# Kernel optimization log

Measured on AMD Instinct MI355X. Metric: run time of the kernel, lower is better.

## Reference

```python
import jax, jax.numpy as jnp
import numpy as np

T, B, E, H = 2048, 2, 1024, 16
D = E // H
NEG = -1e18


def setup_inputs() -> dict:
    key = jax.random.key(0)
    k1, k2, k3, k4, k5 = jax.random.split(key, 5)
    return {
        "query": jax.random.normal(k1, (T, B, E), dtype=jnp.float32),
        "in_proj_weight": jax.random.normal(k2, (3 * E, E), dtype=jnp.float32) * 0.02,
        "in_proj_bias": jax.random.normal(k3, (3 * E,), dtype=jnp.float32) * 0.02,
        "out_proj_weight": jax.random.normal(k4, (E, E), dtype=jnp.float32) * 0.02,
        "out_proj_bias": jax.random.normal(k5, (E,), dtype=jnp.float32) * 0.02,
    }


def reference(query, in_proj_weight, in_proj_bias, out_proj_weight, out_proj_bias):
    # Self-attention (qkv_same), mask_future_timesteps=True, no padding mask,
    # eval mode (dropout p=0), need_weights=True.
    tgt_len, bsz, embed_dim = query.shape
    # fused in-projection: [T,B,3E]
    qkv = jnp.einsum("tbe,fe->tbf", query, in_proj_weight) + in_proj_bias
    q, k, v = jnp.split(qkv, 3, axis=-1)
    q = q * (D ** -0.5)
    # [T,B,E] -> [B*H, T, D]
    def to_heads(x):
        return x.reshape(tgt_len, bsz * H, D).transpose(1, 0, 2)
    q, k, v = to_heads(q), to_heads(k), to_heads(v)
    # scores: [B*H, T, T]
    scores = jnp.einsum("ntd,nsd->nts", q, k)
    causal = jnp.triu(jnp.full((tgt_len, tgt_len), NEG, dtype=scores.dtype), k=1)
    scores = scores + causal[None, :, :]
    attn_weights = jax.nn.softmax(scores, axis=-1)
    # context: [B*H, T, D] -> [T, B, E]
    ctx = jnp.einsum("nts,nsd->ntd", attn_weights, v)
    ctx = ctx.transpose(1, 0, 2).reshape(tgt_len, bsz, embed_dim)
    out = jnp.einsum("tbe,fe->tbf", ctx, out_proj_weight) + out_proj_bias
    # averaged attention weights over heads: [B, T, T]
    avg_w = attn_weights.reshape(bsz, H, tgt_len, tgt_len).sum(axis=1) / H
    return (out, avg_w)
```

## Files before the change

kernel.cpp:

```cpp
#include <hip/hip_runtime.h>
#include <math.h>

#define T_LEN 2048
#define BSZ 2
#define EMB 1024
#define NHEAD 16
#define HDIM 64
#define QK_LD 2048

typedef __attribute__((ext_vector_type(8))) short short8v;
typedef __attribute__((ext_vector_type(4))) float floatx4;

__device__ __forceinline__ short f2bf(float f) {
    unsigned u = __float_as_uint(f);
    u += 0x7fffu + ((u >> 16) & 1u);
    return (short)(u >> 16);
}

__device__ __forceinline__ void async16(const short* g, short* l) {
    __builtin_amdgcn_global_load_lds(
        (const __attribute__((address_space(1))) void*)g,
        (__attribute__((address_space(3))) void*)l, 16, 0, 0);
}

__global__ __launch_bounds__(256) void f32_to_bf16_k(const float* __restrict__ src,
                                                     short* __restrict__ dst, int n) {
    int i = (blockIdx.x * 256 + threadIdx.x) * 4;
    if (i >= n) return;
    float4 v = *(const float4*)(src + i);
    short4 o = make_short4(f2bf(v.x), f2bf(v.y), f2bf(v.z), f2bf(v.w));
    *(short4*)(dst + i) = o;
}

__global__ __launch_bounds__(256) void gemm_bf16(const short* __restrict__ A,
        const short* __restrict__ B, const float* __restrict__ bias,
        void* __restrict__ Cout, short* __restrict__ vTout,
        int M, int N, int K, int scale_cols, int out_bf16, int ldC) {
    __shared__ short As[128][32];
    __shared__ short Bs[128][32];
    const int tid = threadIdx.x;
    const int m0 = blockIdx.x * 128, n0 = blockIdx.y * 128;
    const int lane = tid & 63, w = tid >> 6;
    const int q = lane >> 4, r = lane & 15;
    const int wr = w >> 1, wc = w & 1;

    const int srow = lane >> 2;
    const int spos = lane & 3;
    const int rowL = w * 16 + srow;
    const int rowH = 64 + rowL;
    const int csrc = spos ^ ((rowL >> 1) & 3);
    const short* gA0 = A + (size_t)(m0 + rowL) * K + csrc * 8;
    const short* gA1 = A + (size_t)(m0 + rowH) * K + csrc * 8;
    const short* gB0 = B + (size_t)(n0 + rowL) * K + csrc * 8;
    const short* gB1 = B + (size_t)(n0 + rowH) * K + csrc * 8;
    short* lA0 = &As[w * 16][0];
    short* lA1 = &As[64 + w * 16][0];
    short* lB0 = &Bs[w * 16][0];
    short* lB1 = &Bs[64 + w * 16][0];

    floatx4 acc[4][4];
    #pragma unroll
    for (int a = 0; a < 4; ++a)
        #pragma unroll
        for (int b2 = 0; b2 < 4; ++b2)
            #pragma unroll
            for (int e = 0; e < 4; ++e) acc[a][b2][e] = 0.f;

    for (int k0 = 0; k0 < K; k0 += 32) {
        __syncthreads();
        async16(gA0 + k0, lA0);
        async16(gA1 + k0, lA1);
        async16(gB0 + k0, lB0);
        async16(gB1 + k0, lB1);
        __syncthreads();
        short8v af[4], bfr[4];
        #pragma unroll
        for (int mb = 0; mb < 4; ++mb) {
            int row = wr * 64 + mb * 16 + r;
            af[mb] = *(const short8v*)&As[row][(q ^ ((row >> 1) & 3)) * 8];
        }
        #pragma unroll
        for (int nb = 0; nb < 4; ++nb) {
            int row = wc * 64 + nb * 16 + r;
            bfr[nb] = *(const short8v*)&Bs[row][(q ^ ((row >> 1) & 3)) * 8];
        }
        #pragma unroll
        for (int mb = 0; mb < 4; ++mb)
            #pragma unroll
            for (int nb = 0; nb < 4; ++nb)
                acc[mb][nb] = __builtin_amdgcn_mfma_f32_16x16x32_bf16(af[mb], bfr[nb], acc[mb][nb], 0, 0, 0);
    }

    #pragma unroll
    for (int nb = 0; nb < 4; ++nb) {
        const int col = n0 + wc * 64 + nb * 16 + r;
        const float bi = bias[col];
        const float sc = (col < scale_cols) ? 0.125f : 1.0f;
        if (vTout && col >= 2 * EMB) {
            const int e = col - 2 * EMB;
            #pragma unroll
            for (int mb = 0; mb < 4; ++mb) {
                const int base = m0 + wr * 64 + mb * 16 + q * 4;
                float v0 = acc[mb][nb][0] + bi, v1 = acc[mb][nb][1] + bi;
                float v2 = acc[mb][nb][2] + bi, v3 = acc[mb][nb][3] + bi;
                unsigned lo = (unsigned short)f2bf(v0) | ((unsigned)(unsigned short)f2bf(v2) << 16);
                unsigned hi = (unsigned short)f2bf(v1) | ((unsigned)(unsigned short)f2bf(v3) << 16);
                *(unsigned*)&vTout[(size_t)e * T_LEN + (base >> 1)]         = lo;
                *(unsigned*)&vTout[((size_t)EMB + e) * T_LEN + (base >> 1)] = hi;
            }
        } else {
            #pragma unroll
            for (int mb = 0; mb < 4; ++mb)
                #pragma unroll
                for (int i = 0; i < 4; ++i) {
                    const int rowg = m0 + wr * 64 + mb * 16 + q * 4 + i;
                    const float v = (acc[mb][nb][i] + bi) * sc;
                    if (out_bf16) ((short*)Cout)[(size_t)rowg * ldC + col] = f2bf(v);
                    else          ((float*)Cout)[(size_t)rowg * ldC + col] = v;
                }
        }
    }
}

__global__ __launch_bounds__(256) void flash_fwd(const short* __restrict__ qk,
        const short* __restrict__ vT, short* __restrict__ ctx,
        float* __restrict__ Lr) {
    __shared__ short Ks[128][64];
    __shared__ short Vt[64][128];
    __shared__ short Ps[2][64][64];
    __shared__ float Lred[4][64];
    const int tid = threadIdx.x;
    const int bh = blockIdx.x;
    const int tt = 31 - blockIdx.y;
    const int t0 = tt << 6;
    const int b = bh >> 4, h = bh & 15;
    const int lane = tid & 63, w = tid >> 6;
    const int q = lane >> 4, r = lane & 15;
    const int RS = BSZ * QK_LD;

    const short* qbase = qk + (size_t)b * QK_LD + h * HDIM;
    const short* kbase = qbase + EMB;
    const short* vbase = vT + ((size_t)b * EMB + h * HDIM) * T_LEN;

    const int krow0 = w * 32 + (lane >> 3);
    const short* kg = kbase + (size_t)krow0 * RS + ((lane & 7) ^ (krow0 & 7)) * 8;
    const int vrow0 = w * 16 + (lane >> 4);
    const short* vg[4];
    #pragma unroll
    for (int j = 0; j < 4; ++j) {
        const int vr = vrow0 + j * 4;
        const int gc = ((lane & 15) & 8) | (((lane & 15) & 7) ^ (vr & 7));
        vg[j] = vbase + (size_t)vr * T_LEN + gc * 8;
    }

    {
        const int sr = tid >> 3, c8 = tid & 7;
        *(int4*)&Ps[0][sr][(c8 ^ (sr & 7)) * 8] =
            *(const int4*)(qbase + (size_t)(t0 + sr) * RS + c8 * 8);
        *(int4*)&Ps[0][sr + 32][(c8 ^ ((sr + 32) & 7)) * 8] =
            *(const int4*)(qbase + (size_t)(t0 + sr + 32) * RS + c8 * 8);
    }
    __syncthreads();
    short8v qf[4][2];
    #pragma unroll
    for (int mb = 0; mb < 4; ++mb)
        #pragma unroll
        for (int ks = 0; ks < 2; ++ks) {
            int row = mb * 16 + r;
            qf[mb][ks] = *(const short8v*)&Ps[0][row][((ks * 4 + q) ^ (row & 7)) * 8];
        }

    float l_part[4][4];
    floatx4 o[4];
    #pragma unroll
    for (int mb = 0; mb < 4; ++mb)
        #pragma unroll
        for (int i = 0; i < 4; ++i) l_part[mb][i] = 0.f;
    #pragma unroll
    for (int nb = 0; nb < 4; ++nb)
        #pragma unroll
        for (int e = 0; e < 4; ++e) o[nb][e] = 0.f;

    const int ntiles = tt + 1;
    int s2 = 0;
    for (; s2 + 2 <= ntiles; s2 += 2) {
        __syncthreads();
        {
            const short* kgr = kg + (size_t)(s2 * 64) * RS;
            #pragma unroll
            for (int j = 0; j < 4; ++j)
                async16(kgr + (size_t)(j * 8) * RS, &Ks[w * 32 + j * 8][0]);
            #pragma unroll
            for (int j = 0; j < 4; ++j)
                async16(vg[j] + s2 * 64, &Vt[w * 16 + j * 4][0]);
        }
        __syncthreads();
        #pragma unroll
        for (int t2 = 0; t2 < 2; ++t2) {
            floatx4 sf[4];
            #pragma unroll
            for (int mb = 0; mb < 4; ++mb)
                #pragma unroll
                for (int e = 0; e < 4; ++e) sf[mb][e] = 0.f;
            #pragma unroll
            for (int ks = 0; ks < 2; ++ks) {
                const int krow = t2 * 64 + w * 16 + r;
                short8v kf = *(const short8v*)&Ks[krow][((ks * 4 + q) ^ (krow & 7)) * 8];
                #pragma unroll
                for (int mb = 0; mb < 4; ++mb)
                    sf[mb] = __builtin_amdgcn_mfma_f32_16x16x32_bf16(qf[mb][ks], kf, sf[mb], 0, 0, 0);
            }
            const bool diag = (s2 + t2 == tt);
            #pragma unroll
            for (int mb = 0; mb < 4; ++mb)
                #pragma unroll
                for (int i = 0; i < 4; ++i) {
                    const int rl = mb * 16 + q * 4 + i;
                    float p = (diag && (w * 16 + r > rl)) ? 0.f : __expf(sf[mb][i]);
                    l_part[mb][i] += p;
                    const int c = (w * 2 + (r >> 3)) ^ (rl & 7);
                    Ps[t2][rl][c * 8 + (r & 7)] = f2bf(p);
                }
        }
        __syncthreads();
        #pragma unroll
        for (int ks = 0; ks < 2; ++ks) {
            const int prow = w * 16 + r;
            const int pcp = ((ks * 4 + q) ^ (prow & 7)) * 8;
            short8v pfA = *(const short8v*)&Ps[0][prow][pcp];
            short8v pfB = *(const short8v*)&Ps[1][prow][pcp];
            #pragma unroll
            for (int nb = 0; nb < 4; ++nb) {
                const int vrow = nb * 16 + r;
                const int pcv = (ks * 4 + q) ^ (vrow & 7);
                short8v vfA = *(const short8v*)&Vt[vrow][pcv * 8];
                short8v vfB = *(const short8v*)&Vt[vrow][(8 | pcv) * 8];
                o[nb] = __builtin_amdgcn_mfma_f32_16x16x32_bf16(pfA, vfA, o[nb], 0, 0, 0);
                o[nb] = __builtin_amdgcn_mfma_f32_16x16x32_bf16(pfB, vfB, o[nb], 0, 0, 0);
            }
        }
    }
    if (s2 < ntiles) {
        __syncthreads();
        {
            const int sr = tid >> 2, cb = (tid & 3) * 2;
            const short* kp = kbase + (size_t)(s2 * 64 + sr) * RS;
            const short* vp = vbase + (size_t)sr * T_LEN + s2 * 64;
            #pragma unroll
            for (int u = 0; u < 2; ++u) {
                const int c = cb + u;
                *(int4*)&Ks[sr][(c ^ (sr & 7)) * 8] = *(const int4*)(kp + c * 8);
                *(int4*)&Vt[sr][(c ^ (sr & 7)) * 8] = *(const int4*)(vp + c * 8);
            }
        }
        __syncthreads();
        floatx4 sf[4];
        #pragma unroll
        for (int mb = 0; mb < 4; ++mb)
            #pragma unroll
            for (int e = 0; e < 4; ++e) sf[mb][e] = 0.f;
        #pragma unroll
        for (int ks = 0; ks < 2; ++ks) {
            const int krow = w * 16 + r;
            short8v kf = *(const short8v*)&Ks[krow][((ks * 4 + q) ^ (krow & 7)) * 8];
            #pragma unroll
            for (int mb = 0; mb < 4; ++mb)
                sf[mb] = __builtin_amdgcn_mfma_f32_16x16x32_bf16(qf[mb][ks], kf, sf[mb], 0, 0, 0);
        }
        #pragma unroll
        for (int mb = 0; mb < 4; ++mb)
            #pragma unroll
            for (int i = 0; i < 4; ++i) {
                const int rl = mb * 16 + q * 4 + i;
                float p = (w * 16 + r > rl) ? 0.f : __expf(sf[mb][i]);
                l_part[mb][i] += p;
                const int c = (w * 2 + (r >> 3)) ^ (rl & 7);
                Ps[0][rl][c * 8 + (r & 7)] = f2bf(p);
            }
        __syncthreads();
        #pragma unroll
        for (int ks = 0; ks < 2; ++ks) {
            const int prow = w * 16 + r;
            short8v pf = *(const short8v*)&Ps[0][prow][((ks * 4 + q) ^ (prow & 7)) * 8];
            #pragma unroll
            for (int nb = 0; nb < 4; ++nb) {
                const int vrow = nb * 16 + r;
                short8v vf = *(const short8v*)&Vt[vrow][(((ks * 4 + q) ^ (vrow & 7))) * 8];
                o[nb] = __builtin_amdgcn_mfma_f32_16x16x32_bf16(pf, vf, o[nb], 0, 0, 0);
            }
        }
    }

    #pragma unroll
    for (int mb = 0; mb < 4; ++mb)
        #pragma unroll
        for (int i = 0; i < 4; ++i) {
            float v = l_part[mb][i];
            v += __shfl_xor(v, 1, 16);
            v += __shfl_xor(v, 2, 16);
            v += __shfl_xor(v, 4, 16);
            v += __shfl_xor(v, 8, 16);
            if (r == 0) Lred[w][mb * 16 + q * 4 + i] = v;
        }
    __syncthreads();
    if (tid < 64) {
        float s = Lred[0][tid] + Lred[1][tid] + Lred[2][tid] + Lred[3][tid];
        Lr[(size_t)bh * T_LEN + t0 + tid] = s;
        Lred[0][tid] = s;
    }
    __syncthreads();
    #pragma unroll
    for (int i = 0; i < 4; ++i) {
        const int tl = w * 16 + q * 4 + i;
        const float inv = 1.0f / Lred[0][tl];
        #pragma unroll
        for (int nb = 0; nb < 4; ++nb)
            ctx[((size_t)(t0 + tl) * BSZ + b) * EMB + h * HDIM + nb * 16 + r] =
                f2bf(o[nb][i] * inv);
    }
}

__global__ __launch_bounds__(256) void avg_w_k(const short* __restrict__ qk,
        const float* __restrict__ Lr, float* __restrict__ avg) {
    const int s0 = blockIdx.x * 64, t0 = blockIdx.y * 64, b = blockIdx.z;
    const int tid = threadIdx.x;
    float* outb = avg + (size_t)b * T_LEN * T_LEN;
    if (s0 > t0) {
        const int ty = tid >> 4, tx = tid & 15;
        const float4 z = make_float4(0.f, 0.f, 0.f, 0.f);
        #pragma unroll
        for (int i = 0; i < 4; ++i)
            *(float4*)&outb[(size_t)(t0 + ty * 4 + i) * T_LEN + s0 + tx * 4] = z;
        return;
    }
    __shared__ short Qs[64][128];
    __shared__ short Ks[64][128];
    __shared__ float Lbuf[NHEAD][64];
    const int lane = tid & 63, w = tid >> 6;
    const int q = lane >> 4, r = lane & 15;
    const short* qbase = qk + (size_t)b * QK_LD;
    const int RS = BSZ * QK_LD;

    #pragma unroll
    for (int u = 0; u < 4; ++u) {
        const int li = tid * 4 + u;
        const int h = li >> 6, tl = li & 63;
        Lbuf[h][tl] = 0.0625f / Lr[(size_t)(b * NHEAD + h) * T_LEN + t0 + tl];
    }

    const short* qg[4]; const short* kg[4];
    #pragma unroll
    for (int j = 0; j < 4; ++j) {
        const int row = w * 16 + j * 4 + (lane >> 4);
        const int c = lane & 15;
        const int gc = (c & 8) | ((c & 7) ^ (row & 7));
        qg[j] = qbase + (size_t)(t0 + row) * RS + gc * 8;
        kg[j] = qbase + EMB + (size_t)(s0 + row) * RS + gc * 8;
    }

    floatx4 acc[4];
    #pragma unroll
    for (int nb = 0; nb < 4; ++nb)
        #pragma unroll
        for (int e = 0; e < 4; ++e) acc[nb][e] = 0.f;

    for (int hp = 0; hp < 8; ++hp) {
        __syncthreads();
        #pragma unroll
        for (int j = 0; j < 4; ++j)
            async16(qg[j] + hp * 128, &Qs[w * 16 + j * 4][0]);
        #pragma unroll
        for (int j = 0; j < 4; ++j)
            async16(kg[j] + hp * 128, &Ks[w * 16 + j * 4][0]);
        __syncthreads();

        #pragma unroll
        for (int hs = 0; hs < 2; ++hs) {
            const int h = hp * 2 + hs;
            floatx4 sf[4];
            #pragma unroll
            for (int nb = 0; nb < 4; ++nb)
                #pragma unroll
                for (int e = 0; e < 4; ++e) sf[nb][e] = 0.f;
            #pragma unroll
            for (int ks = 0; ks < 2; ++ks) {
                const int qrow = w * 16 + r;
                short8v qfr = *(const short8v*)
                    &Qs[qrow][((hs * 8) | ((ks * 4 + q) ^ (qrow & 7))) * 8];
                #pragma unroll
                for (int nb = 0; nb < 4; ++nb) {
                    const int krow = nb * 16 + r;
                    short8v kfr = *(const short8v*)
                        &Ks[krow][((hs * 8) | ((ks * 4 + q) ^ (krow & 7))) * 8];
                    sf[nb] = __builtin_amdgcn_mfma_f32_16x16x32_bf16(qfr, kfr, sf[nb], 0, 0, 0);
                }
            }
            #pragma unroll
            for (int i = 0; i < 4; ++i) {
                const int tl = w * 16 + q * 4 + i;
                const float inv = Lbuf[h][tl];
                #pragma unroll
                for (int nb = 0; nb < 4; ++nb) {
                    float e = (s0 == t0 && (nb * 16 + r > tl))
                              ? 0.f : __expf(sf[nb][i]) * inv;
                    acc[nb][i] += e;
                }
            }
        }
    }

    #pragma unroll
    for (int i = 0; i < 4; ++i) {
        const int t = t0 + w * 16 + q * 4 + i;
        #pragma unroll
        for (int nb = 0; nb < 4; ++nb)
            outb[(size_t)t * T_LEN + s0 + nb * 16 + r] = acc[nb][i];
    }
}

extern "C" void kernel_launch(void* const* d_in, const int* in_sizes, int n_in,
                              void* d_out, int out_size, void* d_ws, size_t ws_size,
                              hipStream_t stream) {
    (void)in_sizes; (void)n_in; (void)out_size; (void)ws_size;
    const float* query = (const float*)d_in[0];
    const float* w_in  = (const float*)d_in[1];
    const float* b_in  = (const float*)d_in[2];
    const float* w_out = (const float*)d_in[3];
    const float* b_out = (const float*)d_in[4];

    float* out = (float*)d_out;
    float* avg = out + (size_t)T_LEN * BSZ * EMB;

    short* ws     = (short*)d_ws;
    short* wb_in  = ws;
    short* wb_out = wb_in  + (size_t)3072 * 1024;
    short* qkb    = wb_out + (size_t)1024 * 1024;
    short* vTb    = qkb    + (size_t)4096 * 2048;
    short* ctxb   = vTb    + (size_t)BSZ * EMB * T_LEN;
    float* Lr     = (float*)(ctxb + (size_t)4096 * 1024);
    short* qb     = ctxb;

    f32_to_bf16_k<<<4096, 256, 0, stream>>>(query, qb,     4096 * 1024);
    f32_to_bf16_k<<<3072, 256, 0, stream>>>(w_in,  wb_in,  3072 * 1024);
    f32_to_bf16_k<<<1024, 256, 0, stream>>>(w_out, wb_out, 1024 * 1024);

    gemm_bf16<<<dim3(32, 24), 256, 0, stream>>>(qb, wb_in, b_in, qkb, vTb,
                                                4096, 3072, 1024, EMB, 1, QK_LD);
    flash_fwd<<<dim3(32, 32), 256, 0, stream>>>(qkb, vTb, ctxb, Lr);
    avg_w_k<<<dim3(32, 32, 2), 256, 0, stream>>>(qkb, Lr, avg);
    gemm_bf16<<<dim3(32, 8), 256, 0, stream>>>(ctxb, wb_out, b_out, out, (short*)0,
                                               4096, 1024, 1024, 0, 0, 1024);
}
```

Before: 236.1 us.

## Keep P in registers in flash attention via transposed S and split-K PV

The flash kernel now computes S transposed (K as the A operand) so each lane's score outputs form a ready bf16 A-fragment for a 16x16x16 MFMA with V. The probabilities no longer round-trip through shared memory, which removes the Ps buffer and one barrier per tile pair. Each wave now accumulates a partial O over its own key slice for all 64 query rows, so O registers grow fourfold and a cross-wave reduction through LDS is added at the end. The PV product also moves to smaller-K MFMA instructions, so more MFMA issues are needed per tile.

```diff
diff --git a/kernel.cpp b/kernel.cpp
--- a/kernel.cpp
+++ b/kernel.cpp
@@ -9,6 +9,7 @@
 #define QK_LD 2048
 
 typedef __attribute__((ext_vector_type(8))) short short8v;
+typedef __attribute__((ext_vector_type(4))) short short4v;
 typedef __attribute__((ext_vector_type(4))) float floatx4;
 
 __device__ __forceinline__ short f2bf(float f) {
@@ -16,6 +17,17 @@
     u += 0x7fffu + ((u >> 16) & 1u);
     return (short)(u >> 16);
 }
+
+#if __has_builtin(__builtin_amdgcn_mfma_f32_16x16x16bf16_1k)
+#define MFMA16(a, b, c) __builtin_amdgcn_mfma_f32_16x16x16bf16_1k(a, b, c, 0, 0, 0)
+#else
+__device__ __forceinline__ floatx4 mfma16_asm(short4v a, short4v b, floatx4 c) {
+    floatx4 d;
+    asm("v_mfma_f32_16x16x16_bf16 %0, %1, %2, %3" : "=v"(d) : "v"(a), "v"(b), "v"(c));
+    return d;
+}
+#define MFMA16(a, b, c) mfma16_asm(a, b, c)
+#endif
 
 __device__ __forceinline__ void async16(const short* g, short* l) {
     __builtin_amdgcn_global_load_lds(
@@ -125,9 +137,8 @@
 __global__ __launch_bounds__(256) void flash_fwd(const short* __restrict__ qk,
         const short* __restrict__ vT, short* __restrict__ ctx,
         float* __restrict__ Lr) {
-    __shared__ short Ks[128][64];
-    __shared__ short Vt[64][128];
-    __shared__ short Ps[2][64][64];
+    __shared__ __align__(16) short Ks[128][64];
+    __shared__ __align__(16) short Vt[64][128];
     __shared__ float Lred[4][64];
     const int tid = threadIdx.x;
     const int bh = blockIdx.x;
@@ -155,9 +166,9 @@
 
     {
         const int sr = tid >> 3, c8 = tid & 7;
-        *(int4*)&Ps[0][sr][(c8 ^ (sr & 7)) * 8] =
+        *(int4*)&Ks[sr][(c8 ^ (sr & 7)) * 8] =
             *(const int4*)(qbase + (size_t)(t0 + sr) * RS + c8 * 8);
-        *(int4*)&Ps[0][sr + 32][(c8 ^ ((sr + 32) & 7)) * 8] =
+        *(int4*)&Ks[sr + 32][(c8 ^ ((sr + 32) & 7)) * 8] =
             *(const int4*)(qbase + (size_t)(t0 + sr + 32) * RS + c8 * 8);
     }
     __syncthreads();
@@ -167,19 +178,19 @@
         #pragma unroll
         for (int ks = 0; ks < 2; ++ks) {
             int row = mb * 16 + r;
-            qf[mb][ks] = *(const short8v*)&Ps[0][row][((ks * 4 + q) ^ (row & 7)) * 8];
-        }
-
-    float l_part[4][4];
-    floatx4 o[4];
+            qf[mb][ks] = *(const short8v*)&Ks[row][((ks * 4 + q) ^ (row & 7)) * 8];
+        }
+
+    float l_part[4] = {0.f, 0.f, 0.f, 0.f};
+    floatx4 o[4][4];
     #pragma unroll
     for (int mb = 0; mb < 4; ++mb)
         #pragma unroll
-        for (int i = 0; i < 4; ++i) l_part[mb][i] = 0.f;
-    #pragma unroll
-    for (int nb = 0; nb < 4; ++nb)
-        #pragma unroll
-        for (int e = 0; e < 4; ++e) o[nb][e] = 0.f;
+        for (int nb = 0; nb < 4; ++nb)
+            #pragma unroll
+            for (int e = 0; e < 4; ++e) o[mb][nb][e] = 0.f;
+
+    const int voffbase = (((w * 2 + (q >> 1)) ^ (r & 7)) * 8) + (q & 1) * 4;
 
     const int ntiles = tt + 1;
     int s2 = 0;
@@ -197,46 +208,34 @@
         __syncthreads();
         #pragma unroll
         for (int t2 = 0; t2 < 2; ++t2) {
-            floatx4 sf[4];
-            #pragma unroll
-            for (int mb = 0; mb < 4; ++mb)
-                #pragma unroll
-                for (int e = 0; e < 4; ++e) sf[mb][e] = 0.f;
-            #pragma unroll
-            for (int ks = 0; ks < 2; ++ks) {
-                const int krow = t2 * 64 + w * 16 + r;
-                short8v kf = *(const short8v*)&Ks[krow][((ks * 4 + q) ^ (krow & 7)) * 8];
-                #pragma unroll
-                for (int mb = 0; mb < 4; ++mb)
-                    sf[mb] = __builtin_amdgcn_mfma_f32_16x16x32_bf16(qf[mb][ks], kf, sf[mb], 0, 0, 0);
-            }
+            const int krow = t2 * 64 + w * 16 + r;
+            const int ksw = krow & 7;
+            short8v kf0 = *(const short8v*)&Ks[krow][(q ^ ksw) * 8];
+            short8v kf1 = *(const short8v*)&Ks[krow][((4 + q) ^ ksw) * 8];
+            short4v vf[4];
+            #pragma unroll
+            for (int nb = 0; nb < 4; ++nb)
+                vf[nb] = *(const short4v*)&Vt[nb * 16 + r][t2 * 64 + voffbase];
             const bool diag = (s2 + t2 == tt);
             #pragma unroll
-            for (int mb = 0; mb < 4; ++mb)
-                #pragma unroll
-                for (int i = 0; i < 4; ++i) {
-                    const int rl = mb * 16 + q * 4 + i;
-                    float p = (diag && (w * 16 + r > rl)) ? 0.f : __expf(sf[mb][i]);
-                    l_part[mb][i] += p;
-                    const int c = (w * 2 + (r >> 3)) ^ (rl & 7);
-                    Ps[t2][rl][c * 8 + (r & 7)] = f2bf(p);
-                }
-        }
-        __syncthreads();
-        #pragma unroll
-        for (int ks = 0; ks < 2; ++ks) {
-            const int prow = w * 16 + r;
-            const int pcp = ((ks * 4 + q) ^ (prow & 7)) * 8;
-            short8v pfA = *(const short8v*)&Ps[0][prow][pcp];
-            short8v pfB = *(const short8v*)&Ps[1][prow][pcp];
-            #pragma unroll
-            for (int nb = 0; nb < 4; ++nb) {
-                const int vrow = nb * 16 + r;
-                const int pcv = (ks * 4 + q) ^ (vrow & 7);
-                short8v vfA = *(const short8v*)&Vt[vrow][pcv * 8];
-                short8v vfB = *(const short8v*)&Vt[vrow][(8 | pcv) * 8];
-                o[nb] = __builtin_amdgcn_mfma_f32_16x16x32_bf16(pfA, vfA, o[nb], 0, 0, 0);
-                o[nb] = __builtin_amdgcn_mfma_f32_16x16x32_bf16(pfB, vfB, o[nb], 0, 0, 0);
+            for (int mb = 0; mb < 4; ++mb) {
+                floatx4 sf;
+                #pragma unroll
+                for (int e = 0; e < 4; ++e) sf[e] = 0.f;
+                sf = __builtin_amdgcn_mfma_f32_16x16x32_bf16(kf0, qf[mb][0], sf, 0, 0, 0);
+                sf = __builtin_amdgcn_mfma_f32_16x16x32_bf16(kf1, qf[mb][1], sf, 0, 0, 0);
+                const int t_in = mb * 16 + r;
+                const int s_in = w * 16 + q * 4;
+                float p0 = (diag && (s_in + 0 > t_in)) ? 0.f : __expf(sf[0]);
+                float p1 = (diag && (s_in + 1 > t_in)) ? 0.f : __expf(sf[1]);
+                float p2 = (diag && (s_in + 2 > t_in)) ? 0.f : __expf(sf[2]);
+                float p3 = (diag && (s_in + 3 > t_in)) ? 0.f : __expf(sf[3]);
+                l_part[mb] += (p0 + p1) + (p2 + p3);
+                short4v pa;
+                pa[0] = f2bf(p0); pa[1] = f2bf(p1); pa[2] = f2bf(p2); pa[3] = f2bf(p3);
+                #pragma unroll
+                for (int nb = 0; nb < 4; ++nb)
+                    o[mb][nb] = MFMA16(pa, vf[nb], o[mb][nb]);
             }
         }
     }
@@ -254,69 +253,76 @@
             }
         }
         __syncthreads();
-        floatx4 sf[4];
-        #pragma unroll
-        for (int mb = 0; mb < 4; ++mb)
-            #pragma unroll
-            for (int e = 0; e < 4; ++e) sf[mb][e] = 0.f;
-        #pragma unroll
-        for (int ks = 0; ks < 2; ++ks) {
-            const int krow = w * 16 + r;
-            short8v kf = *(const short8v*)&Ks[krow][((ks * 4 + q) ^ (krow & 7)) * 8];
-            #pragma unroll
-            for (int mb = 0; mb < 4; ++mb)
-                sf[mb] = __builtin_amdgcn_mfma_f32_16x16x32_bf16(qf[mb][ks], kf, sf[mb], 0, 0, 0);
-        }
-        #pragma unroll
-        for (int mb = 0; mb < 4; ++mb)
-            #pragma unroll
-            for (int i = 0; i < 4; ++i) {
-                const int rl = mb * 16 + q * 4 + i;
-                float p = (w * 16 + r > rl) ? 0.f : __expf(sf[mb][i]);
-                l_part[mb][i] += p;
-                const int c = (w * 2 + (r >> 3)) ^ (rl & 7);
-                Ps[0][rl][c * 8 + (r & 7)] = f2bf(p);
-            }
-        __syncthreads();
-        #pragma unroll
-        for (int ks = 0; ks < 2; ++ks) {
-            const int prow = w * 16 + r;
-            short8v pf = *(const short8v*)&Ps[0][prow][((ks * 4 + q) ^ (prow & 7)) * 8];
-            #pragma unroll
-            for (int nb = 0; nb < 4; ++nb) {
-                const int vrow = nb * 16 + r;
-                short8v vf = *(const short8v*)&Vt[vrow][(((ks * 4 + q) ^ (vrow & 7))) * 8];
-                o[nb] = __builtin_amdgcn_mfma_f32_16x16x32_bf16(pf, vf, o[nb], 0, 0, 0);
-            }
-        }
-    }
-
-    #pragma unroll
-    for (int mb = 0; mb < 4; ++mb)
-        #pragma unroll
-        for (int i = 0; i < 4; ++i) {
-            float v = l_part[mb][i];
-            v += __shfl_xor(v, 1, 16);
-            v += __shfl_xor(v, 2, 16);
-            v += __shfl_xor(v, 4, 16);
-            v += __shfl_xor(v, 8, 16);
-            if (r == 0) Lred[w][mb * 16 + q * 4 + i] = v;
-        }
+        const int krow = w * 16 + r;
+        const int ksw = krow & 7;
+        short8v kf0 = *(const short8v*)&Ks[krow][(q ^ ksw) * 8];
+        short8v kf1 = *(const short8v*)&Ks[krow][((4 + q) ^ ksw) * 8];
+        short4v vf[4];
+        #pragma unroll
+        for (int nb = 0; nb < 4; ++nb)
+            vf[nb] = *(const short4v*)&Vt[nb * 16 + r][voffbase];
+        #pragma unroll
+        for (int mb = 0; mb < 4; ++mb) {
+            floatx4 sf;
+            #pragma unroll
+            for (int e = 0; e < 4; ++e) sf[e] = 0.f;
+            sf = __builtin_amdgcn_mfma_f32_16x16x32_bf16(kf0, qf[mb][0], sf, 0, 0, 0);
+            sf = __builtin_amdgcn_mfma_f32_16x16x32_bf16(kf1, qf[mb][1], sf, 0, 0, 0);
+            const int t_in = mb * 16 + r;
+            const int s_in = w * 16 + q * 4;
+            float p0 = (s_in + 0 > t_in) ? 0.f : __expf(sf[0]);
+            float p1 = (s_in + 1 > t_in) ? 0.f : __expf(sf[1]);
+            float p2 = (s_in + 2 > t_in) ? 0.f : __expf(sf[2]);
+            float p3 = (s_in + 3 > t_in) ? 0.f : __expf(sf[3]);
+            l_part[mb] += (p0 + p1) + (p2 + p3);
+            short4v pa;
+            pa[0] = f2bf(p0); pa[1] = f2bf(p1); pa[2] = f2bf(p2); pa[3] = f2bf(p3);
+            #pragma unroll
+            for (int nb = 0; nb < 4; ++nb)
+                o[mb][nb] = MFMA16(pa, vf[nb], o[mb][nb]);
+        }
+    }
+
+    #pragma unroll
+    for (int mb = 0; mb < 4; ++mb) {
+        float v = l_part[mb];
+        v += __shfl_xor(v, 16);
+        v += __shfl_xor(v, 32);
+        if (q == 0) Lred[w][mb * 16 + r] = v;
+    }
     __syncthreads();
     if (tid < 64) {
         float s = Lred[0][tid] + Lred[1][tid] + Lred[2][tid] + Lred[3][tid];
         Lr[(size_t)bh * T_LEN + t0 + tid] = s;
-        Lred[0][tid] = s;
+        Lred[0][tid] = 1.0f / s;
     }
     __syncthreads();
-    #pragma unroll
-    for (int i = 0; i < 4; ++i) {
-        const int tl = w * 16 + q * 4 + i;
-        const float inv = 1.0f / Lred[0][tl];
-        #pragma unroll
-        for (int nb = 0; nb < 4; ++nb)
-            ctx[((size_t)(t0 + tl) * BSZ + b) * EMB + h * HDIM + nb * 16 + r] =
-                f2bf(o[nb][i] * inv);
+
+    float* OA = (float*)&Ks[0][0];
+    float* OB = (float*)&Vt[0][0];
+    float* myO = ((w < 2) ? OA : OB) + (size_t)(w & 1) * (64 * 20);
+    const int tr = tid >> 2, d4 = (tid & 3) * 4;
+    const float inv = Lred[0][tr];
+    short* cbase = ctx + ((size_t)(t0 + tr) * BSZ + b) * EMB + h * HDIM + d4;
+    #pragma unroll
+    for (int nb = 0; nb < 4; ++nb) {
+        #pragma unroll
+        for (int mb = 0; mb < 4; ++mb)
+            #pragma unroll
+            for (int i = 0; i < 4; ++i)
+                myO[(mb * 16 + q * 4 + i) * 20 + r] = o[mb][nb][i];
+        __syncthreads();
+        float4 va = *(float4*)&OA[tr * 20 + d4];
+        float4 vb = *(float4*)&OA[64 * 20 + tr * 20 + d4];
+        float4 vc = *(float4*)&OB[tr * 20 + d4];
+        float4 vd = *(float4*)&OB[64 * 20 + tr * 20 + d4];
+        float v0 = (va.x + vb.x + vc.x + vd.x) * inv;
+        float v1 = (va.y + vb.y + vc.y + vd.y) * inv;
+        float v2 = (va.z + vb.z + vc.z + vd.z) * inv;
+        float v3 = (va.w + vb.w + vc.w + vd.w) * inv;
+        short4 pk = make_short4(f2bf(v0), f2bf(v1), f2bf(v2), f2bf(v3));
+        *(short4*)(cbase + nb * 16) = pk;
+        if (nb < 3) __syncthreads();
     }
 }
 
```

Result: no change. 236.9 us (+0.3%).
